# Performance work log

Measured on AMD Instinct MI355X. Metric: run time of the kernel, lower is better.

## Reference

```python
import jax, jax.numpy as jnp
import numpy as np

B, C, N, K = 4, 192, 8192, 16
C_OUT = 192


def _gather_nodes(xs, idx):
    # xs: [B, C, N], idx: [B, N, K] -> [B, C, N, K]
    return jax.vmap(lambda xb, ib: xb[:, ib])(xs, idx)


def setup_inputs() -> dict:
    key = jax.random.key(0)
    k1, k2, k3 = jax.random.split(key, 3)
    x = jax.random.normal(k1, (B, C, N, 1), dtype=jnp.float32)
    x_0 = jnp.zeros((B, C, N, 1), dtype=jnp.float32)  # unused by forward, kept for interface
    edge_index = jax.random.randint(k2, (2, B, N, K), 0, N, dtype=jnp.int32)
    # 1x1 Conv2d(2C -> C_OUT) weight flattened to [C_OUT, 2C]
    W = jax.random.normal(k3, (C_OUT, 2 * C), dtype=jnp.float32) / np.sqrt(2 * C)
    b = jnp.zeros((C_OUT,), dtype=jnp.float32)
    return {"x": x, "x_0": x_0, "edge_index": edge_index, "W": W, "b": b}


def reference(x, x_0, edge_index, W, b):
    xs = x[..., 0]                       # [B, C, N]
    x_i = _gather_nodes(xs, edge_index[1])   # centers  [B, C, N, K]
    x_j = _gather_nodes(xs, edge_index[0])   # neighbors [B, C, N, K]
    rel = jnp.max(x_j - x_i, axis=-1)        # max-relative [B, C, N]
    y = jnp.concatenate([xs, rel], axis=1)   # [B, 2C, N]
    out = jnp.einsum('oc,bcn->bon', W, y) + b[None, :, None]  # 1x1 conv
    out = jax.nn.relu(out)
    return out[..., None]                # [B, C_OUT, N, 1]
```

## Files before the change

kernel.cpp:

```cpp
#include <hip/hip_runtime.h>

#define B_    4
#define C_    192
#define N_    8192
#define K_    16
#define O_    192
#define TWOC_ 384

typedef __attribute__((ext_vector_type(8))) short short8;
typedef __attribute__((ext_vector_type(4))) short short4v;
typedef __attribute__((ext_vector_type(2))) unsigned int uint2v;
typedef __attribute__((ext_vector_type(4))) float floatx4;

static __device__ __forceinline__ float bf2f(unsigned int u16) {
    union { unsigned int i; float f; } v; v.i = u16 << 16; return v.f;
}
static __device__ __forceinline__ unsigned short f2bf(float f) {
    union { float f; unsigned int i; } v; v.f = f;
    unsigned int x = v.i;
    return (unsigned short)((x + 0x7FFFu + ((x >> 16) & 1u)) >> 16);
}

__global__ __launch_bounds__(256) void k_convert_w(const float* __restrict__ W,
                                                   unsigned short* __restrict__ Wb) {
    int i = blockIdx.x * 256 + threadIdx.x;
    if (i < O_ * TWOC_) Wb[i] = f2bf(W[i]);
}

__global__ __launch_bounds__(256) void k_transpose(const float* __restrict__ x,
                                                   unsigned short* __restrict__ xt) {
    __shared__ float tile[32][33];
    int bid  = blockIdx.x;
    int xcd  = bid & 7;
    int b    = xcd >> 1;
    int half = xcd & 1;
    int slot = bid >> 3;
    int ct   = slot >> 7;
    int nt   = half * 128 + (slot & 127);
    int c0 = ct * 32, n0 = nt * 32;
    int tid = threadIdx.x;

    int cc  = tid >> 3;
    int nn4 = (tid & 7) * 4;
    const float* xp = x + ((size_t)b * C_ + c0 + cc) * N_ + n0 + nn4;
    float4 v = *(const float4*)xp;
    tile[nn4 + 0][cc] = v.x;
    tile[nn4 + 1][cc] = v.y;
    tile[nn4 + 2][cc] = v.z;
    tile[nn4 + 3][cc] = v.w;
    __syncthreads();

#pragma unroll
    for (int i = 0; i < 2; i++) {
        int id  = i * 256 + tid;
        int row = id >> 4;
        int ch2 = id & 15;
        float a = tile[row][ch2 * 2];
        float c = tile[row][ch2 * 2 + 1];
        unsigned int pack = (unsigned int)f2bf(a) | ((unsigned int)f2bf(c) << 16);
        *(unsigned int*)(xt + ((size_t)b * N_ + n0 + row) * C_ + c0 + ch2 * 2) = pack;
    }
}

__global__ __launch_bounds__(256) void k_fused(const unsigned short* __restrict__ xt,
                                               const int* __restrict__ eidx,
                                               const unsigned short* __restrict__ Wb,
                                               const float* __restrict__ bias,
                                               float* __restrict__ out) {
    __shared__ unsigned short ytile[64][TWOC_];
    __shared__ int sidx[64][33];

    int bid  = blockIdx.x;
    int xcd  = bid & 7;
    int b    = xcd >> 1;
    int slot = bid >> 3;
    int n0   = ((xcd & 1) * 64 + slot) * 64;

    int tid  = threadIdx.x;
    int wave = tid >> 6;
    int lane = tid & 63;

    const int* e0 = eidx + ((size_t)b * N_ + n0) * K_;
    const int* e1 = e0 + (size_t)B_ * N_ * K_;
#pragma unroll
    for (int i = 0; i < 4; i++) {
        int id   = i * 256 + tid;
        int node = id >> 4, k = id & 15;
        sidx[node][k]      = e0[id];
        sidx[node][16 + k] = e1[id];
    }

    const unsigned short* xrow = xt + ((size_t)b * N_ + n0) * C_;
#pragma unroll
    for (int i = 0; i < 6; i++) {
        int id = i * 256 + tid;
        int row = id / 24, chunk = id % 24;
        short8 v = *(const short8*)(xrow + (size_t)row * C_ + chunk * 8);
        *(short8*)&ytile[row][chunk * 8] = v;
    }
    __syncthreads();

    {
        int g  = lane >> 4;
        int l4 = lane & 15;
        const unsigned short* xbase = xt + (size_t)b * N_ * C_;
#pragma unroll
        for (int bb = 0; bb < 4; bb++) {
            int node = wave * 16 + bb * 4 + g;
            float m[3][4];
#pragma unroll
            for (int t = 0; t < 3; t++)
#pragma unroll
                for (int c = 0; c < 4; c++) m[t][c] = -INFINITY;
#pragma unroll
            for (int k = 0; k < K_; k++) {
                int jn = sidx[node][k];
                int in = sidx[node][16 + k];
                const unsigned short* pj = xbase + (size_t)jn * C_ + l4 * 4;
                const unsigned short* pi = xbase + (size_t)in * C_ + l4 * 4;
#pragma unroll
                for (int t = 0; t < 3; t++) {
                    uint2v vj = *(const uint2v*)(pj + t * 64);
                    uint2v vi = *(const uint2v*)(pi + t * 64);
                    m[t][0] = fmaxf(m[t][0], bf2f(vj.x & 0xffffu) - bf2f(vi.x & 0xffffu));
                    m[t][1] = fmaxf(m[t][1], bf2f(vj.x >> 16)     - bf2f(vi.x >> 16));
                    m[t][2] = fmaxf(m[t][2], bf2f(vj.y & 0xffffu) - bf2f(vi.y & 0xffffu));
                    m[t][3] = fmaxf(m[t][3], bf2f(vj.y >> 16)     - bf2f(vi.y >> 16));
                }
            }
#pragma unroll
            for (int t = 0; t < 3; t++) {
                short4v s;
                s.x = (short)f2bf(m[t][0]);
                s.y = (short)f2bf(m[t][1]);
                s.z = (short)f2bf(m[t][2]);
                s.w = (short)f2bf(m[t][3]);
                *(short4v*)&ytile[node][C_ + t * 64 + l4 * 4] = s;
            }
        }
    }
    __syncthreads();

    int m16  = lane & 15;
    int quad = lane >> 4;
    const unsigned short* wbase = Wb + (size_t)(wave * 48 + m16) * TWOC_ + quad * 8;

    floatx4 acc[3][4];
#pragma unroll
    for (int i = 0; i < 3; i++)
#pragma unroll
        for (int j = 0; j < 4; j++) acc[i][j] = (floatx4){0.f, 0.f, 0.f, 0.f};

#pragma unroll 2
    for (int kt = 0; kt < 12; kt++) {
        short8 wf[3], yf[4];
#pragma unroll
        for (int i = 0; i < 3; i++)
            wf[i] = *(const short8*)(wbase + (size_t)(i * 16) * TWOC_ + kt * 32);
#pragma unroll
        for (int j = 0; j < 4; j++)
            yf[j] = *(const short8*)&ytile[j * 16 + m16][kt * 32 + quad * 8];
#pragma unroll
        for (int i = 0; i < 3; i++)
#pragma unroll
            for (int j = 0; j < 4; j++)
                acc[i][j] = __builtin_amdgcn_mfma_f32_16x16x32_bf16(wf[i], yf[j], acc[i][j], 0, 0, 0);
    }

#pragma unroll
    for (int i = 0; i < 3; i++) {
#pragma unroll
        for (int r = 0; r < 4; r++) {
            int o = wave * 48 + i * 16 + quad * 4 + r;
            float bv = bias[o];
#pragma unroll
            for (int j = 0; j < 4; j++) {
                int n = n0 + j * 16 + m16;
                out[((size_t)b * O_ + o) * N_ + n] = fmaxf(acc[i][j][r] + bv, 0.f);
            }
        }
    }
}

extern "C" void kernel_launch(void* const* d_in, const int* in_sizes, int n_in,
                              void* d_out, int out_size, void* d_ws, size_t ws_size,
                              hipStream_t stream) {
    const float* x    = (const float*)d_in[0];
    const int*   eidx = (const int*)d_in[2];
    const float* W    = (const float*)d_in[3];
    const float* bias = (const float*)d_in[4];
    float*       out  = (float*)d_out;

    unsigned short* Wb = (unsigned short*)d_ws;
    unsigned short* xt = (unsigned short*)((char*)d_ws + 147456);

    k_convert_w<<<dim3((O_ * TWOC_ + 255) / 256), dim3(256), 0, stream>>>(W, Wb);
    k_transpose<<<dim3(6144), dim3(256), 0, stream>>>(x, xt);
    k_fused<<<dim3(512), dim3(256), 0, stream>>>(xt, eidx, Wb, bias, out);
}
```

Measured before the change: 134.0 us.

## Switch to fp16 packed max, halve node tile, split GEMM around gather

Converts activations and weights from bf16 to fp16 so the max-relative gather can use packed half-precision subtract and max instead of per-element unpack to fp32. The node tile per block drops from 64 to 32 and the grid doubles, shrinking LDS to raise occupancy. The x half of the 1x1 conv is now computed directly from global memory before the gather, and only the relative half goes through an XOR-swizzled LDS tile. fp16 narrows the dynamic range compared with bf16, and the -65504 initial max value is used in place of negative infinity.

```diff
diff --git a/kernel.cpp b/kernel.cpp
--- a/kernel.cpp
+++ b/kernel.cpp
@@ -1,4 +1,5 @@
 #include <hip/hip_runtime.h>
+#include <hip/hip_fp16.h>
 
 #define B_    4
 #define C_    192
@@ -7,24 +8,20 @@
 #define O_    192
 #define TWOC_ 384
 
-typedef __attribute__((ext_vector_type(8))) short short8;
-typedef __attribute__((ext_vector_type(4))) short short4v;
-typedef __attribute__((ext_vector_type(2))) unsigned int uint2v;
+typedef __attribute__((ext_vector_type(8))) _Float16 half8;
+typedef __attribute__((ext_vector_type(4))) _Float16 half4v;
 typedef __attribute__((ext_vector_type(4))) float floatx4;
 
-static __device__ __forceinline__ float bf2f(unsigned int u16) {
-    union { unsigned int i; float f; } v; v.i = u16 << 16; return v.f;
-}
-static __device__ __forceinline__ unsigned short f2bf(float f) {
-    union { float f; unsigned int i; } v; v.f = f;
-    unsigned int x = v.i;
-    return (unsigned short)((x + 0x7FFFu + ((x >> 16) & 1u)) >> 16);
-}
+#define NINF ((_Float16)(-65504.0f))
 
 __global__ __launch_bounds__(256) void k_convert_w(const float* __restrict__ W,
                                                    unsigned short* __restrict__ Wb) {
     int i = blockIdx.x * 256 + threadIdx.x;
-    if (i < O_ * TWOC_) Wb[i] = f2bf(W[i]);
+    if (i < O_ * TWOC_) {
+        union { _Float16 h; unsigned short s; } v;
+        v.h = (_Float16)W[i];
+        Wb[i] = v.s;
+    }
 }
 
 __global__ __launch_bounds__(256) void k_transpose(const float* __restrict__ x,
@@ -55,116 +52,116 @@
         int id  = i * 256 + tid;
         int row = id >> 4;
         int ch2 = id & 15;
-        float a = tile[row][ch2 * 2];
-        float c = tile[row][ch2 * 2 + 1];
-        unsigned int pack = (unsigned int)f2bf(a) | ((unsigned int)f2bf(c) << 16);
-        *(unsigned int*)(xt + ((size_t)b * N_ + n0 + row) * C_ + c0 + ch2 * 2) = pack;
+        union { _Float16 h[2]; unsigned int u; } p;
+        p.h[0] = (_Float16)tile[row][ch2 * 2];
+        p.h[1] = (_Float16)tile[row][ch2 * 2 + 1];
+        *(unsigned int*)(xt + ((size_t)b * N_ + n0 + row) * C_ + c0 + ch2 * 2) = p.u;
     }
 }
 
-__global__ __launch_bounds__(256) void k_fused(const unsigned short* __restrict__ xt,
-                                               const int* __restrict__ eidx,
-                                               const unsigned short* __restrict__ Wb,
-                                               const float* __restrict__ bias,
-                                               float* __restrict__ out) {
-    __shared__ unsigned short ytile[64][TWOC_];
-    __shared__ int sidx[64][33];
+__global__ __launch_bounds__(256, 4) void k_fused(const unsigned short* __restrict__ xt,
+                                                  const int* __restrict__ eidx,
+                                                  const unsigned short* __restrict__ Wb,
+                                                  const float* __restrict__ bias,
+                                                  float* __restrict__ out) {
+    __shared__ __align__(16) unsigned short rtile[32][192];
+    __shared__ int sidx[32][33];
 
     int bid  = blockIdx.x;
     int xcd  = bid & 7;
     int b    = xcd >> 1;
     int slot = bid >> 3;
-    int n0   = ((xcd & 1) * 64 + slot) * 64;
+    int n0   = ((xcd & 1) * 128 + slot) * 32;
 
     int tid  = threadIdx.x;
     int wave = tid >> 6;
     int lane = tid & 63;
+    int m16  = lane & 15;
+    int quad = lane >> 4;
 
     const int* e0 = eidx + ((size_t)b * N_ + n0) * K_;
     const int* e1 = e0 + (size_t)B_ * N_ * K_;
 #pragma unroll
-    for (int i = 0; i < 4; i++) {
-        int id   = i * 256 + tid;
+    for (int i = 0; i < 2; i++) {
+        int id = i * 256 + tid;
         int node = id >> 4, k = id & 15;
         sidx[node][k]      = e0[id];
         sidx[node][16 + k] = e1[id];
     }
 
-    const unsigned short* xrow = xt + ((size_t)b * N_ + n0) * C_;
+    floatx4 acc[3][2];
 #pragma unroll
-    for (int i = 0; i < 6; i++) {
-        int id = i * 256 + tid;
-        int row = id / 24, chunk = id % 24;
-        short8 v = *(const short8*)(xrow + (size_t)row * C_ + chunk * 8);
-        *(short8*)&ytile[row][chunk * 8] = v;
+    for (int i = 0; i < 3; i++)
+#pragma unroll
+        for (int j = 0; j < 2; j++) acc[i][j] = (floatx4){0.f, 0.f, 0.f, 0.f};
+
+    const unsigned short* wbase = Wb + (size_t)(wave * 48 + m16) * TWOC_ + quad * 8;
+    const unsigned short* ybase = xt + ((size_t)b * N_ + n0 + m16) * C_ + quad * 8;
+
+#pragma unroll 2
+    for (int kt = 0; kt < 6; kt++) {
+        half8 wf[3], yf[2];
+#pragma unroll
+        for (int i = 0; i < 3; i++)
+            wf[i] = *(const half8*)(wbase + (size_t)(i * 16) * TWOC_ + kt * 32);
+#pragma unroll
+        for (int j = 0; j < 2; j++)
+            yf[j] = *(const half8*)(ybase + (size_t)(j * 16) * C_ + kt * 32);
+#pragma unroll
+        for (int i = 0; i < 3; i++)
+#pragma unroll
+            for (int j = 0; j < 2; j++)
+                acc[i][j] = __builtin_amdgcn_mfma_f32_16x16x32_f16(wf[i], yf[j], acc[i][j], 0, 0, 0);
     }
+
     __syncthreads();
 
     {
-        int g  = lane >> 4;
-        int l4 = lane & 15;
         const unsigned short* xbase = xt + (size_t)b * N_ * C_;
+        int g = quad, l4 = m16;
 #pragma unroll
-        for (int bb = 0; bb < 4; bb++) {
-            int node = wave * 16 + bb * 4 + g;
-            float m[3][4];
-#pragma unroll
-            for (int t = 0; t < 3; t++)
-#pragma unroll
-                for (int c = 0; c < 4; c++) m[t][c] = -INFINITY;
+        for (int bb = 0; bb < 2; bb++) {
+            int node = wave * 8 + bb * 4 + g;
+            half8  m0 = {NINF, NINF, NINF, NINF, NINF, NINF, NINF, NINF};
+            half4v m1 = {NINF, NINF, NINF, NINF};
 #pragma unroll
             for (int k = 0; k < K_; k++) {
-                int jn = sidx[node][k];
-                int in = sidx[node][16 + k];
-                const unsigned short* pj = xbase + (size_t)jn * C_ + l4 * 4;
-                const unsigned short* pi = xbase + (size_t)in * C_ + l4 * 4;
-#pragma unroll
-                for (int t = 0; t < 3; t++) {
-                    uint2v vj = *(const uint2v*)(pj + t * 64);
-                    uint2v vi = *(const uint2v*)(pi + t * 64);
-                    m[t][0] = fmaxf(m[t][0], bf2f(vj.x & 0xffffu) - bf2f(vi.x & 0xffffu));
-                    m[t][1] = fmaxf(m[t][1], bf2f(vj.x >> 16)     - bf2f(vi.x >> 16));
-                    m[t][2] = fmaxf(m[t][2], bf2f(vj.y & 0xffffu) - bf2f(vi.y & 0xffffu));
-                    m[t][3] = fmaxf(m[t][3], bf2f(vj.y >> 16)     - bf2f(vi.y >> 16));
-                }
+                int jn  = sidx[node][k];
+                int in_ = sidx[node][16 + k];
+                const unsigned short* pj = xbase + (size_t)jn * C_;
+                const unsigned short* pi = xbase + (size_t)in_ * C_;
+                half8  a0 = *(const half8*)(pj + l4 * 8);
+                half8  b0 = *(const half8*)(pi + l4 * 8);
+                half4v a1 = *(const half4v*)(pj + 128 + l4 * 4);
+                half4v b1 = *(const half4v*)(pi + 128 + l4 * 4);
+                m0 = __builtin_elementwise_max(m0, a0 - b0);
+                m1 = __builtin_elementwise_max(m1, a1 - b1);
             }
-#pragma unroll
-            for (int t = 0; t < 3; t++) {
-                short4v s;
-                s.x = (short)f2bf(m[t][0]);
-                s.y = (short)f2bf(m[t][1]);
-                s.z = (short)f2bf(m[t][2]);
-                s.w = (short)f2bf(m[t][3]);
-                *(short4v*)&ytile[node][C_ + t * 64 + l4 * 4] = s;
-            }
+            char* rb = (char*)rtile + node * 384;
+            unsigned int sw = (unsigned)(node & 7) << 4;
+            *(half8*)(rb + ((unsigned)(l4 * 16) ^ sw))        = m0;
+            *(half4v*)(rb + ((unsigned)(256 + l4 * 8) ^ sw))  = m1;
         }
     }
     __syncthreads();
 
-    int m16  = lane & 15;
-    int quad = lane >> 4;
-    const unsigned short* wbase = Wb + (size_t)(wave * 48 + m16) * TWOC_ + quad * 8;
-
-    floatx4 acc[3][4];
-#pragma unroll
-    for (int i = 0; i < 3; i++)
-#pragma unroll
-        for (int j = 0; j < 4; j++) acc[i][j] = (floatx4){0.f, 0.f, 0.f, 0.f};
-
 #pragma unroll 2
-    for (int kt = 0; kt < 12; kt++) {
-        short8 wf[3], yf[4];
+    for (int kt = 0; kt < 6; kt++) {
+        half8 wf[3], yf[2];
 #pragma unroll
         for (int i = 0; i < 3; i++)
-            wf[i] = *(const short8*)(wbase + (size_t)(i * 16) * TWOC_ + kt * 32);
+            wf[i] = *(const half8*)(wbase + (size_t)(i * 16) * TWOC_ + (C_ + kt * 32));
 #pragma unroll
-        for (int j = 0; j < 4; j++)
-            yf[j] = *(const short8*)&ytile[j * 16 + m16][kt * 32 + quad * 8];
+        for (int j = 0; j < 2; j++) {
+            int r = j * 16 + m16;
+            unsigned int off = (unsigned)(kt * 64 + quad * 16) ^ ((unsigned)(r & 7) << 4);
+            yf[j] = *(const half8*)((char*)rtile + (size_t)r * 384 + off);
+        }
 #pragma unroll
         for (int i = 0; i < 3; i++)
 #pragma unroll
-            for (int j = 0; j < 4; j++)
-                acc[i][j] = __builtin_amdgcn_mfma_f32_16x16x32_bf16(wf[i], yf[j], acc[i][j], 0, 0, 0);
+            for (int j = 0; j < 2; j++)
+                acc[i][j] = __builtin_amdgcn_mfma_f32_16x16x32_f16(wf[i], yf[j], acc[i][j], 0, 0, 0);
     }
 
 #pragma unroll
@@ -174,7 +171,7 @@
             int o = wave * 48 + i * 16 + quad * 4 + r;
             float bv = bias[o];
 #pragma unroll
-            for (int j = 0; j < 4; j++) {
+            for (int j = 0; j < 2; j++) {
                 int n = n0 + j * 16 + m16;
                 out[((size_t)b * O_ + o) * N_ + n] = fmaxf(acc[i][j][r] + bv, 0.f);
             }
@@ -196,5 +193,5 @@
 
     k_convert_w<<<dim3((O_ * TWOC_ + 255) / 256), dim3(256), 0, stream>>>(W, Wb);
     k_transpose<<<dim3(6144), dim3(256), 0, stream>>>(x, xt);
-    k_fused<<<dim3(512), dim3(256), 0, stream>>>(xt, eidx, Wb, bias, out);
+    k_fused<<<dim3(1024), dim3(256), 0, stream>>>(xt, eidx, Wb, bias, out);
 }
```

Measured after the change: 139.3 us. +3.9%, slower.
